# Kernel optimization log

Measured on AMD Instinct MI355X. Metric: run time of the kernel, lower is better.

The kernel has to match this reference:

```python
import jax, jax.numpy as jnp
import numpy as np

N = 50000          # num nodes
E = 800000         # num edges
DIN = 128          # in_channels
C = 64             # out_channels per head
H = 2              # heads
ED = 32            # edge_dim


def setup_inputs() -> dict:
    key = jax.random.key(0)
    ks = jax.random.split(key, 12)
    s = 1.0 / np.sqrt(DIN)
    se = 1.0 / np.sqrt(ED)
    return {
        "x": jax.random.normal(ks[0], (N, DIN), dtype=jnp.float32),
        "edge_index": jax.random.randint(ks[1], (2, E), 0, N, dtype=jnp.int32),
        "edge_attr": jax.random.normal(ks[2], (E, ED), dtype=jnp.float32),
        "Wq": jax.random.uniform(ks[3], (DIN, H * C), jnp.float32, -s, s),
        "bq": jax.random.uniform(ks[4], (H * C,), jnp.float32, -s, s),
        "Wk": jax.random.uniform(ks[5], (DIN, H * C), jnp.float32, -s, s),
        "bk": jax.random.uniform(ks[6], (H * C,), jnp.float32, -s, s),
        "Wv": jax.random.uniform(ks[7], (DIN, H * C), jnp.float32, -s, s),
        "bv": jax.random.uniform(ks[8], (H * C,), jnp.float32, -s, s),
        "We": jax.random.uniform(ks[9], (ED, H * C), jnp.float32, -se, se),
        "Wskip": jax.random.uniform(ks[10], (DIN, H * C), jnp.float32, -s, s),
        "bskip": jax.random.uniform(ks[11], (H * C,), jnp.float32, -s, s),
    }


def reference(x, edge_index, edge_attr, Wq, bq, Wk, bk, Wv, bv, We, Wskip, bskip):
    src, dst = edge_index[0], edge_index[1]
    # node-level projections [N, H, C]
    q = (x @ Wq + bq).reshape(N, H, C)
    k = (x @ Wk + bk).reshape(N, H, C)
    v = (x @ Wv + bv).reshape(N, H, C)
    e = (edge_attr @ We).reshape(E, H, C)  # lin_edge, no bias

    # per-edge gather
    q_e = q[dst]              # [E, H, C]
    k_e = k[src] + e          # key gets edge features
    alpha = jnp.einsum("ehc,ehc->eh", q_e, k_e) / jnp.sqrt(jnp.float32(C))

    # segment softmax over incoming edges of each dst node
    m = jax.ops.segment_max(alpha, dst, num_segments=N)       # [N, H]
    alpha = jnp.exp(alpha - m[dst])
    denom = jax.ops.segment_sum(alpha, dst, num_segments=N)   # [N, H]
    alpha = alpha / (denom[dst] + 1e-16)

    # weighted aggregation of values (value also gets edge features)
    msg = (v[src] + e) * alpha[..., None]                     # [E, H, C]
    out = jax.ops.segment_sum(msg, dst, num_segments=N)       # [N, H, C]
    out = out.reshape(N, H * C)

    # root weight skip connection (concat=True, beta=False)
    return out + x @ Wskip + bskip
```

## Files before the change

### kernel.cpp

```cpp
#include <hip/hip_runtime.h>
#include <cstdint>

#define NN 50000
#define EE 800000
#define DINC 128
#define HC 128
#define EDC 32
#define CAP 56
#define TILES 1563
#define SCAT_BLKS 3125
#define NB_SCAN 196

typedef __attribute__((ext_vector_type(8))) short short8;
typedef __attribute__((ext_vector_type(4))) float floatx4;

__device__ __forceinline__ unsigned int pk2(float a, float b){
  unsigned int ua = __float_as_uint(a), ub = __float_as_uint(b);
  ua = (ua + 0x7FFFu + ((ua >> 16) & 1u)) >> 16;
  ub = (ub + 0x7FFFu + ((ub >> 16) & 1u)) & 0xFFFF0000u;
  return ua | ub;
}
__device__ __forceinline__ float bflo(unsigned int p){ return __uint_as_float(p << 16); }
__device__ __forceinline__ float bfhi(unsigned int p){ return __uint_as_float(p & 0xFFFF0000u); }

__global__ __launch_bounds__(256) void k_prew(
    const float* __restrict__ Wq, const float* __restrict__ Wk,
    const float* __restrict__ Wv, const float* __restrict__ Wsk,
    unsigned int* __restrict__ Wp)
{
  int idx = blockIdx.x*256 + threadIdx.x;
  int mat = idx >> 13;
  int r   = idx & 8191;
  int kp  = r >> 7;
  int n   = r & 127;
  const float* W = (mat==0)?Wq:(mat==1)?Wk:(mat==2)?Wv:Wsk;
  Wp[(mat<<13) + n*64 + kp] = pk2(W[(2*kp)*HC + n], W[(2*kp+1)*HC + n]);
}

__global__ __launch_bounds__(256) void k_fused(
    const float* __restrict__ x, const unsigned int* __restrict__ Wp,
    const float* __restrict__ bq, const float* __restrict__ bk,
    const float* __restrict__ bv, const float* __restrict__ bsk,
    const int* __restrict__ ei,
    unsigned int* __restrict__ qbf, unsigned int* __restrict__ kvb,
    float* __restrict__ out, int* __restrict__ cnt, int* __restrict__ eidl,
    const int do_scatter)
{
  __shared__ unsigned int sx[32*68];

  if (do_scatter && blockIdx.x >= TILES){
    int e = (blockIdx.x - TILES)*256 + threadIdx.x;
    if (e < EE){
      int d = ei[EE + e];
      int pos = atomicAdd(cnt + d, 1);
      if (pos < CAP) eidl[d*CAP + pos] = e;
    }
    return;
  }

  const int tid = threadIdx.x;
  const int bm  = blockIdx.x * 32;

  for (int idx = tid; idx < 32*32; idx += 256){
    int row = idx >> 5, kq = idx & 31;
    int gr = bm + row;
    unsigned int p0 = 0u, p1 = 0u;
    if (gr < NN){
      float4 v = *(const float4*)(x + (size_t)gr*DINC + 4*kq);
      p0 = pk2(v.x, v.y); p1 = pk2(v.z, v.w);
    }
    sx[row*68 + 2*kq]     = p0;
    sx[row*68 + 2*kq + 1] = p1;
  }
  __syncthreads();

  const int l = tid & 63, wid = tid >> 6;
  const int lm = l & 15, ks = l >> 4;
  const int pe = lm & 1;
  const int n0 = wid * 32;

  short8 a_f[4][2];
  #pragma unroll
  for (int kb = 0; kb < 4; ++kb){
    a_f[kb][0] = *(const short8*)(sx + lm*68      + kb*16 + ks*4);
    a_f[kb][1] = *(const short8*)(sx + (16+lm)*68 + kb*16 + ks*4);
  }

  #pragma unroll
  for (int mat = 0; mat < 4; ++mat){
    const unsigned int* wp = Wp + (mat<<13);
    const float* bi = (mat==0)?bq:(mat==1)?bk:(mat==2)?bv:bsk;

    floatx4 acc[2][2];
    #pragma unroll
    for (int mt=0;mt<2;mt++)
      #pragma unroll
      for (int nt=0;nt<2;nt++) acc[mt][nt] = (floatx4){0.f,0.f,0.f,0.f};

    #pragma unroll
    for (int kb = 0; kb < 4; ++kb){
      short8 b0 = *(const short8*)(wp + (n0+lm)*64    + kb*16 + ks*4);
      short8 b1 = *(const short8*)(wp + (n0+16+lm)*64 + kb*16 + ks*4);
      acc[0][0] = __builtin_amdgcn_mfma_f32_16x16x32_bf16(a_f[kb][0], b0, acc[0][0], 0, 0, 0);
      acc[0][1] = __builtin_amdgcn_mfma_f32_16x16x32_bf16(a_f[kb][0], b1, acc[0][1], 0, 0, 0);
      acc[1][0] = __builtin_amdgcn_mfma_f32_16x16x32_bf16(a_f[kb][1], b0, acc[1][0], 0, 0, 0);
      acc[1][1] = __builtin_amdgcn_mfma_f32_16x16x32_bf16(a_f[kb][1], b1, acc[1][1], 0, 0, 0);
    }

    if (mat < 3){
      #pragma unroll
      for (int nt=0; nt<2; ++nt){
        const int cbase = n0 + nt*16 + (lm & ~1);
        float2 bb = *(const float2*)(bi + cbase);
        const int cp = cbase >> 1;
        #pragma unroll
        for (int mt=0; mt<2; ++mt){
          #pragma unroll
          for (int s=0; s<2; ++s){
            float a_even = acc[mt][nt][2*s];
            float a_odd  = acc[mt][nt][2*s+1];
            float sw_even = __shfl_xor(a_even, 1, 64);
            float sw_odd  = __shfl_xor(a_odd,  1, 64);
            float self = pe ? a_odd  : a_even;
            float part = pe ? sw_odd : sw_even;
            float lo = pe ? part : self;
            float hi = pe ? self : part;
            unsigned int pv = pk2(lo + bb.x, hi + bb.y);
            int gr = bm + mt*16 + ks*4 + 2*s + pe;
            if (gr < NN){
              if (mat == 0)      qbf[gr*64 + cp] = pv;
              else if (mat == 1) kvb[(size_t)gr*128 + cp]      = pv;
              else               kvb[(size_t)gr*128 + 64 + cp] = pv;
            }
          }
        }
      }
    } else {
      #pragma unroll
      for (int nt=0; nt<2; ++nt){
        const int col = n0 + nt*16 + lm;
        float bs = bi[col];
        #pragma unroll
        for (int mt=0; mt<2; ++mt){
          #pragma unroll
          for (int r=0; r<4; ++r){
            int gr = bm + mt*16 + ks*4 + r;
            if (gr < NN) out[(size_t)gr*HC + col] = acc[mt][nt][r] + bs;
          }
        }
      }
    }
  }
}

__global__ __launch_bounds__(256) void k_count(const int* __restrict__ ei,
    int* __restrict__ cnt)
{
  int e = blockIdx.x*256 + threadIdx.x;
  if (e < EE) atomicAdd(cnt + ei[EE + e], 1);
}
__global__ __launch_bounds__(256) void k_blksum(const int* __restrict__ cnt,
    int* __restrict__ bsum)
{
  __shared__ int s[256];
  int t = threadIdx.x, i = blockIdx.x*256 + t;
  s[t] = (i < NN) ? cnt[i] : 0;
  __syncthreads();
  for (int d = 128; d > 0; d >>= 1){
    if (t < d) s[t] += s[t + d];
    __syncthreads();
  }
  if (t == 0) bsum[blockIdx.x] = s[0];
}
__global__ __launch_bounds__(256) void k_bscan(const int* __restrict__ bsum,
    int* __restrict__ bpre)
{
  __shared__ int s[256];
  int t = threadIdx.x;
  int v = (t < NB_SCAN) ? bsum[t] : 0;
  s[t] = v;
  __syncthreads();
  for (int d = 1; d < 256; d <<= 1){
    int u = (t >= d) ? s[t - d] : 0;
    __syncthreads();
    s[t] += u;
    __syncthreads();
  }
  if (t < NB_SCAN) bpre[t] = s[t] - v;
}
__global__ __launch_bounds__(256) void k_scan3(const int* __restrict__ cnt,
    const int* __restrict__ bpre, int* __restrict__ off, int* __restrict__ woff)
{
  __shared__ int s[256];
  int t = threadIdx.x, i = blockIdx.x*256 + t;
  int v = (i < NN) ? cnt[i] : 0;
  s[t] = v;
  __syncthreads();
  for (int d = 1; d < 256; d <<= 1){
    int u = (t >= d) ? s[t - d] : 0;
    __syncthreads();
    s[t] += u;
    __syncthreads();
  }
  if (i < NN){
    int o = bpre[blockIdx.x] + s[t] - v;
    off[i] = o; woff[i] = o;
  }
}
__global__ __launch_bounds__(256) void k_scatter(const int* __restrict__ ei,
    int* __restrict__ woff, int* __restrict__ eidl)
{
  int e = blockIdx.x*256 + threadIdx.x;
  if (e < EE){
    int d = ei[EE + e];
    int pos = atomicAdd(woff + d, 1);
    eidl[pos] = e;
  }
}

__global__ __launch_bounds__(256) void k_agg(
    const float* __restrict__ eattr, const float* __restrict__ We,
    const unsigned int* __restrict__ qbf, const unsigned int* __restrict__ kvb,
    const int* __restrict__ ei,
    const int* __restrict__ cnt, const int* __restrict__ off,
    const int* __restrict__ eidl, const int fixed,
    float* __restrict__ out)
{
  __shared__ float sWeT[128*33];
  __shared__ float sWea[256];
  const int tid = threadIdx.x;
  for (int idx = tid; idx < EDC*HC; idx += 256){
    int jj = idx >> 7, col = idx & 127;
    sWeT[col*33 + jj] = We[idx];
  }
  __syncthreads();

  const int wid = tid >> 6, l = tid & 63;
  const int node = blockIdx.x*4 + wid;
  const int h = l >> 5, j = l & 31;

  int deg = cnt[node]; if (deg > CAP) deg = CAP;
  const size_t beg = fixed ? (size_t)node*CAP : (size_t)off[node];
  int eidL = 0, srcL = 0;
  if (deg > 0){
    eidL = eidl[beg + ((l < deg) ? l : 0)];
    srcL = ei[eidL];
  }
  const unsigned int eaOff = (unsigned int)eidL * (EDC*4);
  const unsigned int kOff  = (unsigned int)srcL * 512u;
  const unsigned int jB = (unsigned int)j * 4u;
  const unsigned int lB = (unsigned int)l * 4u;
  const char* eac = (const char*)eattr;
  const char* kvc = (const char*)kvb;

  unsigned int qp = qbf[node*64 + l];
  float q0 = bflo(qp), q1 = bfhi(qp);
  float Pl = 0.f;
  {
    const uint4* qrow4 = (const uint4*)(qbf + node*64 + h*32);
    const float* wt = sWeT + (h*64)*33 + j;
    #pragma unroll
    for (int c4 = 0; c4 < 8; ++c4){
      uint4 u = qrow4[c4];
      int b = 8*c4;
      Pl += bflo(u.x)*wt[(b+0)*33] + bfhi(u.x)*wt[(b+1)*33];
      Pl += bflo(u.y)*wt[(b+2)*33] + bfhi(u.y)*wt[(b+3)*33];
      Pl += bflo(u.z)*wt[(b+4)*33] + bfhi(u.z)*wt[(b+5)*33];
      Pl += bflo(u.w)*wt[(b+6)*33] + bfhi(u.w)*wt[(b+7)*33];
    }
  }

#define GATHER(base, EA, KK, VV)                                 \
  {                                                              \
    _Pragma("unroll")                                            \
    for (int t = 0; t < 4; ++t){                                 \
      int s = (base) + t;                                        \
      int it = (s < deg) ? s : 0;                                \
      unsigned int eo = (unsigned int)__shfl((int)eaOff, it, 64) + jB; \
      unsigned int ko = (unsigned int)__shfl((int)kOff,  it, 64) + lB; \
      EA[t] = *(const float*)(eac + eo);                         \
      KK[t] = *(const unsigned int*)(kvc + ko);                  \
      VV[t] = *(const unsigned int*)(kvc + ko + 256);            \
    }                                                            \
  }

  float acc0=0.f, acc1=0.f, wea=0.f, den=0.f;
  if (deg > 0){
    float eav[4]; unsigned int kk[4], vv[4];
    GATHER(0, eav, kk, vv);

    for (int i = 0; i < deg; i += 4){
      float eavn[4]; unsigned int kkn[4], vvn[4];
      const int inext = i + 4;
      if (inext < deg){
        GATHER(inext, eavn, kkn, vvn);
      }
      float p[4];
      #pragma unroll
      for (int t = 0; t < 4; ++t)
        p[t] = q0*bflo(kk[t]) + q1*bfhi(kk[t]) + Pl*eav[t];
      #pragma unroll
      for (int s = 1; s < 32; s <<= 1){
        #pragma unroll
        for (int t = 0; t < 4; ++t) p[t] += __shfl_xor(p[t], s, 32);
      }
      const int nb = deg - i;
      #pragma unroll
      for (int t = 0; t < 4; ++t){
        float a = __expf(p[t] * 0.125f);
        if (t > 0) a = (t < nb) ? a : 0.f;
        den  += a;
        acc0 += a*bflo(vv[t]);
        acc1 += a*bfhi(vv[t]);
        wea  += a*eav[t];
      }
      #pragma unroll
      for (int t = 0; t < 4; ++t){ eav[t] = eavn[t]; kk[t] = kkn[t]; vv[t] = vvn[t]; }
    }
  }
#undef GATHER

  sWea[tid] = wea;
  __syncthreads();
  float rden = 1.0f/(den + 1e-16f);
  float e0 = 0.f, e1 = 0.f;
  const float* w0 = sWeT + (2*l)*33;
  const float* w1 = sWeT + (2*l+1)*33;
  const float* wv = sWea + wid*64 + h*32;
  #pragma unroll
  for (int jj = 0; jj < 32; jj += 4){
    float4 w4 = *(const float4*)(wv + jj);
    e0 += w4.x*w0[jj]; e1 += w4.x*w1[jj];
    e0 += w4.y*w0[jj+1]; e1 += w4.y*w1[jj+1];
    e0 += w4.z*w0[jj+2]; e1 += w4.z*w1[jj+2];
    e0 += w4.w*w0[jj+3]; e1 += w4.w*w1[jj+3];
  }
  float2 sk = *(const float2*)(out + (size_t)node*HC + 2*l);
  float2 o;
  o.x = sk.x + (acc0 + e0)*rden;
  o.y = sk.y + (acc1 + e1)*rden;
  *(float2*)(out + (size_t)node*HC + 2*l) = o;
}

extern "C" void kernel_launch(void* const* d_in, const int* in_sizes, int n_in,
                              void* d_out, int out_size, void* d_ws, size_t ws_size,
                              hipStream_t stream)
{
  const float* x   = (const float*)d_in[0];
  const int*   ei  = (const int*)d_in[1];
  const float* ea  = (const float*)d_in[2];
  const float* Wq  = (const float*)d_in[3];
  const float* bq  = (const float*)d_in[4];
  const float* Wk  = (const float*)d_in[5];
  const float* bk  = (const float*)d_in[6];
  const float* Wv  = (const float*)d_in[7];
  const float* bv  = (const float*)d_in[8];
  const float* We  = (const float*)d_in[9];
  const float* Wsk = (const float*)d_in[10];
  const float* bsk = (const float*)d_in[11];
  float* out = (float*)d_out;

  char* ws = (char*)d_ws;
  unsigned int* qbf = (unsigned int*)(ws);
  unsigned int* kvb = (unsigned int*)(ws + 12800000);
  int* cnt = (int*)(ws + 38400000);

  hipMemsetAsync(cnt, 0, NN*sizeof(int), stream);

  if (ws_size >= 50000000ull){
    int* eidl = (int*)(ws + 38600000);
    unsigned int* Wp = (unsigned int*)(ws + 49800064);
    k_prew<<<128, 256, 0, stream>>>(Wq, Wk, Wv, Wsk, Wp);
    k_fused<<<TILES + SCAT_BLKS, 256, 0, stream>>>(
        x, Wp, bq, bk, bv, bsk, ei, qbf, kvb, out, cnt, eidl, 1);
    k_agg<<<12500, 256, 0, stream>>>(ea, We, qbf, kvb, ei,
                                     cnt, (const int*)nullptr, eidl, 1, out);
  } else {
    int* off  = (int*)(ws + 38600000);
    int* woff = (int*)(ws + 38800000);
    int* bsum = (int*)(ws + 39000000);
    int* bpre = (int*)(ws + 39001024);
    int* eidl = (int*)(ws + 39002048);
    unsigned int* Wp = (unsigned int*)(ws + 42202112);
    k_prew<<<128, 256, 0, stream>>>(Wq, Wk, Wv, Wsk, Wp);
    k_fused<<<TILES, 256, 0, stream>>>(
        x, Wp, bq, bk, bv, bsk, ei, qbf, kvb, out, cnt, nullptr, 0);
    k_count  <<<SCAT_BLKS, 256, 0, stream>>>(ei, cnt);
    k_blksum <<<NB_SCAN, 256, 0, stream>>>(cnt, bsum);
    k_bscan  <<<1, 256, 0, stream>>>(bsum, bpre);
    k_scan3  <<<NB_SCAN, 256, 0, stream>>>(cnt, bpre, off, woff);
    k_scatter<<<SCAT_BLKS, 256, 0, stream>>>(ei, woff, eidl);
    k_agg<<<12500, 256, 0, stream>>>(ea, We, qbf, kvb, ei,
                                     cnt, off, eidl, 0, out);
  }
}
```

Baseline: 398.1 us.

## Precompute Wq·We projection via MFMA, fold memset into prew, use DPP reductions and exp2

Folds the per-node q·We product into a precomputed combined weight (Wq·We^T plus a bias term). It is computed as an extra MFMA tile inside the fused projection kernel and stored as a per-node float array, so the aggregation kernel just loads it instead of running a 64-term LDS dot product. The counter memset moves into the prew kernel, the 32-lane reductions use DPP instead of shuffles, and the softmax scale is folded into q so exp2 replaces expf. The new path runs only when the workspace is at least 62.8 MB and adds 12.8 MB of extra writes and reads. The precombined weights are rounded to bf16, which adds some error.

```diff
diff --git a/kernel.cpp b/kernel.cpp
--- a/kernel.cpp
+++ b/kernel.cpp
@@ -10,6 +10,7 @@
 #define TILES 1563
 #define SCAT_BLKS 3125
 #define NB_SCAN 196
+#define PREW_GRID (145 + NB_SCAN)
 
 typedef __attribute__((ext_vector_type(8))) short short8;
 typedef __attribute__((ext_vector_type(4))) float floatx4;
@@ -23,27 +24,70 @@
 __device__ __forceinline__ float bflo(unsigned int p){ return __uint_as_float(p << 16); }
 __device__ __forceinline__ float bfhi(unsigned int p){ return __uint_as_float(p & 0xFFFF0000u); }
 
+__device__ __forceinline__ float red32(float r){
+  r += __int_as_float(__builtin_amdgcn_update_dpp(0, __float_as_int(r), 0xB1, 0xF, 0xF, true));
+  r += __int_as_float(__builtin_amdgcn_update_dpp(0, __float_as_int(r), 0x4E, 0xF, 0xF, true));
+  r += __int_as_float(__builtin_amdgcn_update_dpp(0, __float_as_int(r), 0x141, 0xF, 0xF, true));
+  r += __int_as_float(__builtin_amdgcn_update_dpp(0, __float_as_int(r), 0x140, 0xF, 0xF, true));
+  r += __shfl_xor(r, 16, 32);
+  return r;
+}
+
 __global__ __launch_bounds__(256) void k_prew(
     const float* __restrict__ Wq, const float* __restrict__ Wk,
     const float* __restrict__ Wv, const float* __restrict__ Wsk,
-    unsigned int* __restrict__ Wp)
-{
-  int idx = blockIdx.x*256 + threadIdx.x;
-  int mat = idx >> 13;
-  int r   = idx & 8191;
-  int kp  = r >> 7;
-  int n   = r & 127;
-  const float* W = (mat==0)?Wq:(mat==1)?Wk:(mat==2)?Wv:Wsk;
-  Wp[(mat<<13) + n*64 + kp] = pk2(W[(2*kp)*HC + n], W[(2*kp+1)*HC + n]);
+    const float* __restrict__ We, const float* __restrict__ bq,
+    unsigned int* __restrict__ Wp, unsigned int* __restrict__ Wp5,
+    float* __restrict__ Pb, int* __restrict__ cnt)
+{
+  const int b = blockIdx.x, tid = threadIdx.x;
+  if (b < 128){
+    int idx = b*256 + tid;
+    int mat = idx >> 13;
+    int r   = idx & 8191;
+    int kp  = r >> 7;
+    int n   = r & 127;
+    const float* W = (mat==0)?Wq:(mat==1)?Wk:(mat==2)?Wv:Wsk;
+    Wp[(mat<<13) + n*64 + kp] = pk2(W[(2*kp)*HC + n], W[(2*kp+1)*HC + n]);
+  } else if (b < 144){
+    if (!Wp5) return;
+    int t = (b-128)*256 + tid;
+    int kp = t >> 6, n = t & 63;
+    int h = n >> 5, j = n & 31;
+    const float* wq0 = Wq + (2*kp)*HC + h*64;
+    const float* wq1 = wq0 + HC;
+    const float* wer = We + j*HC + h*64;
+    float d0 = 0.f, d1 = 0.f;
+    #pragma unroll 8
+    for (int c = 0; c < 64; ++c){
+      float w = wer[c];
+      d0 += wq0[c]*w; d1 += wq1[c]*w;
+    }
+    Wp5[n*64 + kp] = pk2(d0, d1);
+  } else if (b == 144){
+    if (!Wp5 || tid >= 64) return;
+    int n = tid, h = n >> 5, j = n & 31;
+    const float* wer = We + j*HC + h*64;
+    const float* bqh = bq + h*64;
+    float s = 0.f;
+    #pragma unroll 8
+    for (int c = 0; c < 64; ++c) s += bqh[c]*wer[c];
+    Pb[n] = s;
+  } else {
+    int idx = (b-145)*256 + tid;
+    if (idx < NN) cnt[idx] = 0;
+  }
 }
 
 __global__ __launch_bounds__(256) void k_fused(
     const float* __restrict__ x, const unsigned int* __restrict__ Wp,
+    const unsigned int* __restrict__ Wp5, const float* __restrict__ Pb,
     const float* __restrict__ bq, const float* __restrict__ bk,
     const float* __restrict__ bv, const float* __restrict__ bsk,
     const int* __restrict__ ei,
     unsigned int* __restrict__ qbf, unsigned int* __restrict__ kvb,
-    float* __restrict__ out, int* __restrict__ cnt, int* __restrict__ eidl,
+    float* __restrict__ out, float* __restrict__ Pfl,
+    int* __restrict__ cnt, int* __restrict__ eidl,
     const int do_scatter)
 {
   __shared__ unsigned int sx[32*68];
@@ -151,6 +195,36 @@
       }
     }
   }
+
+  if (Pfl != nullptr && wid < 2){
+    floatx4 acc[2][2];
+    #pragma unroll
+    for (int mt=0;mt<2;mt++)
+      #pragma unroll
+      for (int nt=0;nt<2;nt++) acc[mt][nt] = (floatx4){0.f,0.f,0.f,0.f};
+    #pragma unroll
+    for (int kb = 0; kb < 4; ++kb){
+      short8 b0 = *(const short8*)(Wp5 + (n0+lm)*64    + kb*16 + ks*4);
+      short8 b1 = *(const short8*)(Wp5 + (n0+16+lm)*64 + kb*16 + ks*4);
+      acc[0][0] = __builtin_amdgcn_mfma_f32_16x16x32_bf16(a_f[kb][0], b0, acc[0][0], 0, 0, 0);
+      acc[0][1] = __builtin_amdgcn_mfma_f32_16x16x32_bf16(a_f[kb][0], b1, acc[0][1], 0, 0, 0);
+      acc[1][0] = __builtin_amdgcn_mfma_f32_16x16x32_bf16(a_f[kb][1], b0, acc[1][0], 0, 0, 0);
+      acc[1][1] = __builtin_amdgcn_mfma_f32_16x16x32_bf16(a_f[kb][1], b1, acc[1][1], 0, 0, 0);
+    }
+    #pragma unroll
+    for (int nt=0; nt<2; ++nt){
+      const int col = n0 + nt*16 + lm;
+      float bs = Pb[col];
+      #pragma unroll
+      for (int mt=0; mt<2; ++mt){
+        #pragma unroll
+        for (int r=0; r<4; ++r){
+          int gr = bm + mt*16 + ks*4 + r;
+          if (gr < NN) Pfl[(size_t)gr*64 + col] = acc[mt][nt][r] + bs;
+        }
+      }
+    }
+  }
 }
 
 __global__ __launch_bounds__(256) void k_count(const int* __restrict__ ei,
@@ -223,7 +297,7 @@
     const unsigned int* __restrict__ qbf, const unsigned int* __restrict__ kvb,
     const int* __restrict__ ei,
     const int* __restrict__ cnt, const int* __restrict__ off,
-    const int* __restrict__ eidl, const int fixed,
+    const int* __restrict__ eidl, const int fixed, const float* __restrict__ Pfl,
     float* __restrict__ out)
 {
   __shared__ float sWeT[128*33];
@@ -253,21 +327,26 @@
   const char* eac = (const char*)eattr;
   const char* kvc = (const char*)kvb;
 
+  const float SC = 0.18033688f;
   unsigned int qp = qbf[node*64 + l];
-  float q0 = bflo(qp), q1 = bfhi(qp);
-  float Pl = 0.f;
-  {
+  float q0 = bflo(qp)*SC, q1 = bfhi(qp)*SC;
+  float Pl;
+  if (Pfl != nullptr){
+    Pl = Pfl[(size_t)node*64 + l] * SC;
+  } else {
     const uint4* qrow4 = (const uint4*)(qbf + node*64 + h*32);
     const float* wt = sWeT + (h*64)*33 + j;
+    float s = 0.f;
     #pragma unroll
     for (int c4 = 0; c4 < 8; ++c4){
       uint4 u = qrow4[c4];
       int b = 8*c4;
-      Pl += bflo(u.x)*wt[(b+0)*33] + bfhi(u.x)*wt[(b+1)*33];
-      Pl += bflo(u.y)*wt[(b+2)*33] + bfhi(u.y)*wt[(b+3)*33];
-      Pl += bflo(u.z)*wt[(b+4)*33] + bfhi(u.z)*wt[(b+5)*33];
-      Pl += bflo(u.w)*wt[(b+6)*33] + bfhi(u.w)*wt[(b+7)*33];
-    }
+      s += bflo(u.x)*wt[(b+0)*33] + bfhi(u.x)*wt[(b+1)*33];
+      s += bflo(u.y)*wt[(b+2)*33] + bfhi(u.y)*wt[(b+3)*33];
+      s += bflo(u.z)*wt[(b+4)*33] + bfhi(u.z)*wt[(b+5)*33];
+      s += bflo(u.w)*wt[(b+6)*33] + bfhi(u.w)*wt[(b+7)*33];
+    }
+    Pl = s*SC;
   }
 
 #define GATHER(base, EA, KK, VV)                                 \
@@ -300,14 +379,11 @@
       for (int t = 0; t < 4; ++t)
         p[t] = q0*bflo(kk[t]) + q1*bfhi(kk[t]) + Pl*eav[t];
       #pragma unroll
-      for (int s = 1; s < 32; s <<= 1){
-        #pragma unroll
-        for (int t = 0; t < 4; ++t) p[t] += __shfl_xor(p[t], s, 32);
-      }
+      for (int t = 0; t < 4; ++t) p[t] = red32(p[t]);
       const int nb = deg - i;
       #pragma unroll
       for (int t = 0; t < 4; ++t){
-        float a = __expf(p[t] * 0.125f);
+        float a = __builtin_amdgcn_exp2f(p[t]);
         if (t > 0) a = (t < nb) ? a : 0.f;
         den  += a;
         acc0 += a*bflo(vv[t]);
@@ -365,16 +441,25 @@
   unsigned int* kvb = (unsigned int*)(ws + 12800000);
   int* cnt = (int*)(ws + 38400000);
 
-  hipMemsetAsync(cnt, 0, NN*sizeof(int), stream);
-
-  if (ws_size >= 50000000ull){
+  if (ws_size >= 62800000ull){
+    int* eidl = (int*)(ws + 38600000);
+    unsigned int* Wp  = (unsigned int*)(ws + 49800064);
+    unsigned int* Wp5 = (unsigned int*)(ws + 49931264);
+    float* Pb  = (float*)(ws + 49947648);
+    float* Pfl = (float*)(ws + 49948160);
+    k_prew<<<PREW_GRID, 256, 0, stream>>>(Wq, Wk, Wv, Wsk, We, bq, Wp, Wp5, Pb, cnt);
+    k_fused<<<TILES + SCAT_BLKS, 256, 0, stream>>>(
+        x, Wp, Wp5, Pb, bq, bk, bv, bsk, ei, qbf, kvb, out, Pfl, cnt, eidl, 1);
+    k_agg<<<12500, 256, 0, stream>>>(ea, We, qbf, kvb, ei,
+                                     cnt, (const int*)nullptr, eidl, 1, Pfl, out);
+  } else if (ws_size >= 50000000ull){
     int* eidl = (int*)(ws + 38600000);
     unsigned int* Wp = (unsigned int*)(ws + 49800064);
-    k_prew<<<128, 256, 0, stream>>>(Wq, Wk, Wv, Wsk, Wp);
+    k_prew<<<PREW_GRID, 256, 0, stream>>>(Wq, Wk, Wv, Wsk, We, bq, Wp, nullptr, nullptr, cnt);
     k_fused<<<TILES + SCAT_BLKS, 256, 0, stream>>>(
-        x, Wp, bq, bk, bv, bsk, ei, qbf, kvb, out, cnt, eidl, 1);
+        x, Wp, nullptr, nullptr, bq, bk, bv, bsk, ei, qbf, kvb, out, nullptr, cnt, eidl, 1);
     k_agg<<<12500, 256, 0, stream>>>(ea, We, qbf, kvb, ei,
-                                     cnt, (const int*)nullptr, eidl, 1, out);
+                                     cnt, (const int*)nullptr, eidl, 1, nullptr, out);
   } else {
     int* off  = (int*)(ws + 38600000);
     int* woff = (int*)(ws + 38800000);
@@ -382,15 +467,15 @@
     int* bpre = (int*)(ws + 39001024);
     int* eidl = (int*)(ws + 39002048);
     unsigned int* Wp = (unsigned int*)(ws + 42202112);
-    k_prew<<<128, 256, 0, stream>>>(Wq, Wk, Wv, Wsk, Wp);
+    k_prew<<<PREW_GRID, 256, 0, stream>>>(Wq, Wk, Wv, Wsk, We, bq, Wp, nullptr, nullptr, cnt);
     k_fused<<<TILES, 256, 0, stream>>>(
-        x, Wp, bq, bk, bv, bsk, ei, qbf, kvb, out, cnt, nullptr, 0);
+        x, Wp, nullptr, nullptr, bq, bk, bv, bsk, ei, qbf, kvb, out, nullptr, cnt, nullptr, 0);
     k_count  <<<SCAT_BLKS, 256, 0, stream>>>(ei, cnt);
     k_blksum <<<NB_SCAN, 256, 0, stream>>>(cnt, bsum);
     k_bscan  <<<1, 256, 0, stream>>>(bsum, bpre);
     k_scan3  <<<NB_SCAN, 256, 0, stream>>>(cnt, bpre, off, woff);
     k_scatter<<<SCAT_BLKS, 256, 0, stream>>>(ei, woff, eidl);
     k_agg<<<12500, 256, 0, stream>>>(ea, We, qbf, kvb, ei,
-                                     cnt, off, eidl, 0, out);
-  }
-}
+                                     cnt, off, eidl, 0, nullptr, out);
+  }
+}
```

New measurement: 403.1 us. About the same (+1.2%).
